# Performance work log

Measured on AMD Instinct MI355X. Metric: run time of the kernel, lower is better.

The kernel has to match this reference:

```python
import jax, jax.numpy as jnp
import numpy as np

V_THRESH = 0.3

@jax.custom_vjp
def spike(x):
    return (x > 0).astype(x.dtype)

def _spike_fwd(x):
    return spike(x), x

def _spike_bwd(x, g):
    # rectangular straight-through surrogate gradient (pass grad where |x| < 0.5)
    return (g * (jnp.abs(x) < 0.5).astype(g.dtype),)

spike.defvjp(_spike_fwd, _spike_bwd)


def setup_inputs() -> dict:
    key = jax.random.key(0)
    B, T, H = 128, 2048, 128
    k1, = jax.random.split(key, 1)
    x_seq = jax.random.normal(k1, (B, T, H), dtype=jnp.float32)
    v0 = jnp.zeros((B, H), dtype=jnp.float32)
    z0 = jnp.zeros((B, H), dtype=jnp.float32)
    decay_raw = jnp.zeros((H,), dtype=jnp.float32)  # nn.initializers.constant(0.0)
    return {"x_seq": x_seq, "v0": v0, "z0": z0, "decay_raw": decay_raw}


def reference(x_seq, v0, z0, decay_raw):
    # LIF recurrence: v_t = v_{t-1} * decay * (1 - z_{t-1}) + x_t ; z_t = spike(v_t - v_thresh)
    decay = jax.nn.sigmoid(decay_raw)  # (H,)

    def step(carry, x_t):
        v, z = carry
        v = v * decay * (1.0 - z) + x_t
        z_out = spike(v - V_THRESH)
        return (v, z_out), z_out

    x_tb = jnp.swapaxes(x_seq, 0, 1)  # [T, B, H] for lax.scan over time
    (_, _), spk_tb = jax.lax.scan(step, (v0, z0), x_tb)
    return jnp.swapaxes(spk_tb, 0, 1)  # [B, T, H]
```

## Files before the change

### kernel.cpp

```cpp
#include <hip/hip_runtime.h>
#include <math.h>


constexpr int Bdim = 128;
constexpr int Tdim = 2048;
constexpr int Hdim = 128;
constexpr int HW   = 64;
constexpr int U    = 128;
constexpr int XBUF = 4;
constexpr int NTILE = Tdim / U;
constexpr int NW   = 5;
constexpr float VTH = 0.3f;

typedef const __attribute__((address_space(1))) void* gptr_t;
typedef __attribute__((address_space(3))) void* lptr_t;

#define BAR() asm volatile("s_barrier" ::: "memory")

__global__ __launch_bounds__(NW * 64) void lif_kernel(
    const float* __restrict__ x,
    const float* __restrict__ v0,
    const float* __restrict__ z0,
    const float* __restrict__ decay_raw,
    float* __restrict__ out)
{
    __shared__ float xs[XBUF][U][HW];

    const int tid  = threadIdx.x;
    const int wave = tid >> 6;
    const int lane = tid & 63;
    const int blk  = blockIdx.x;
    const int b    = blk >> 1;
    const int h0   = (blk & 1) * HW;

    const float* xbase = x   + (size_t)b * Tdim * Hdim + h0;
    float*       obase = out + (size_t)b * Tdim * Hdim + h0;

    if (wave == 0) {
        const float decay = 1.0f / (1.0f + expf(-decay_raw[h0 + lane]));
        float v = v0[b * Hdim + h0 + lane];
        float z = z0[b * Hdim + h0 + lane];
        float* ol = obase + lane;

        BAR();

        for (int k = 0; k < NTILE; ++k) {
            const float (*xt)[HW] = xs[k & 3];
            float xa[8], xb[8], zb[8];
            #pragma unroll
            for (int j = 0; j < 8; ++j) xa[j] = xt[j][lane];

            #pragma unroll
            for (int bt = 0; bt < 16; ++bt) {
                if (bt < 15) {
                    #pragma unroll
                    for (int j = 0; j < 8; ++j) {
                        const float t = xt[(bt + 1) * 8 + j][lane];
                        if (bt & 1) xa[j] = t; else xb[j] = t;
                    }
                }
                #pragma unroll
                for (int j = 0; j < 8; ++j) {
                    const float xv = (bt & 1) ? xb[j] : xa[j];
                    const float vd = v * decay;
                    v = ((z > 0.5f) ? 0.0f : vd) + xv;
                    z = (v > VTH) ? 1.0f : 0.0f;
                    zb[j] = z;
                }
                const size_t t0 = (size_t)k * U + bt * 8;
                #pragma unroll
                for (int j = 0; j < 8; ++j)
                    ol[(t0 + j) * Hdim] = zb[j];
            }
            BAR();
        }
    } else {
        const int sub = (lane >> 4) * Hdim + (lane & 15) * 4;

        auto fill = [&](int tile, int buf) {
            const float* g = xbase + (size_t)tile * U * Hdim + sub;
            #pragma unroll
            for (int q = 0; q < 8; ++q) {
                const int jj = (wave - 1) * 8 + q;
                __builtin_amdgcn_global_load_lds(
                    (gptr_t)(const void*)(g + (size_t)(4 * jj) * Hdim),
                    (lptr_t)(void*)&xs[buf][4 * jj][0],
                    16, 0, 0);
            }
        };

        fill(0, 0); fill(1, 1); fill(2, 2);
        asm volatile("s_waitcnt vmcnt(16)" ::: "memory");
        BAR();

        for (int k = 0; k < NTILE; ++k) {
            if (k + 3 < NTILE) {
                fill(k + 3, (k + 3) & 3);
                asm volatile("s_waitcnt vmcnt(16)" ::: "memory");
            } else if (k == NTILE - 3) {
                asm volatile("s_waitcnt vmcnt(8)" ::: "memory");
            } else if (k == NTILE - 2) {
                asm volatile("s_waitcnt vmcnt(0)" ::: "memory");
            }
            BAR();
        }
    }
}

extern "C" void kernel_launch(void* const* d_in, const int* in_sizes, int n_in,
                              void* d_out, int out_size, void* d_ws, size_t ws_size,
                              hipStream_t stream) {
    const float* x         = (const float*)d_in[0];
    const float* v0        = (const float*)d_in[1];
    const float* z0        = (const float*)d_in[2];
    const float* decay_raw = (const float*)d_in[3];
    float* out = (float*)d_out;

    lif_kernel<<<Bdim * Hdim / HW, NW * 64, 0, stream>>>(x, v0, z0, decay_raw, out);
}
```

Before: 249.5 us.

## Offload spike stores to a writer wave via bit-packed LDS handoff

The compute wave no longer issues global stores. It packs each lane's spikes into 32-bit masks in LDS, and a dedicated third wave unpacks them and writes float4 rows to global memory one tile behind. Loading is consolidated into a single producer wave using 64-step tiles across six buffers, which shrinks the block from five waves to three. The aim is to take the scattered 4-byte output stores off the serial recurrence's critical path, at the cost of an extra LDS round-trip and a barrier per tile.

```diff
diff --git a/kernel.cpp b/kernel.cpp
--- a/kernel.cpp
+++ b/kernel.cpp
@@ -6,25 +6,23 @@
 constexpr int Tdim = 2048;
 constexpr int Hdim = 128;
 constexpr int HW   = 64;
-constexpr int U    = 128;
-constexpr int XBUF = 4;
-constexpr int NTILE = Tdim / U;
-constexpr int NW   = 5;
+constexpr int U    = 64;
+constexpr int NB   = 6;
+constexpr int NT   = Tdim / U;
 constexpr float VTH = 0.3f;
 
 typedef const __attribute__((address_space(1))) void* gptr_t;
 typedef __attribute__((address_space(3))) void* lptr_t;
 
-#define BAR() asm volatile("s_barrier" ::: "memory")
-
-__global__ __launch_bounds__(NW * 64) void lif_kernel(
+__global__ __launch_bounds__(192) void lif_kernel(
     const float* __restrict__ x,
     const float* __restrict__ v0,
     const float* __restrict__ z0,
     const float* __restrict__ decay_raw,
     float* __restrict__ out)
 {
-    __shared__ float xs[XBUF][U][HW];
+    __shared__ float    xs[NB][U][HW];
+    __shared__ unsigned zw[2][2][HW];
 
     const int tid  = threadIdx.x;
     const int wave = tid >> 6;
@@ -36,74 +34,94 @@
     const float* xbase = x   + (size_t)b * Tdim * Hdim + h0;
     float*       obase = out + (size_t)b * Tdim * Hdim + h0;
 
-    if (wave == 0) {
-        const float decay = 1.0f / (1.0f + expf(-decay_raw[h0 + lane]));
+    if (wave == 1) {
+        const int sub = (lane >> 4) * Hdim + (lane & 15) * 4;
+        auto fill = [&](int tile, int buf) {
+            const float* g = xbase + (size_t)tile * U * Hdim + sub;
+            #pragma unroll
+            for (int q = 0; q < 16; ++q)
+                __builtin_amdgcn_global_load_lds(
+                    (gptr_t)(const void*)(g + (size_t)(4 * q) * Hdim),
+                    (lptr_t)(void*)&xs[buf][4 * q][0], 16, 0, 0);
+        };
+        fill(0, 0); fill(1, 1); fill(2, 2);
+        asm volatile("s_waitcnt vmcnt(32)");
+        __builtin_amdgcn_s_barrier();
+        int buf = 3;
+        for (int k = 0; k < NT; ++k) {
+            if (k + 3 < NT) {
+                fill(k + 3, buf);
+                buf = (buf + 1 == NB) ? 0 : buf + 1;
+                asm volatile("s_waitcnt vmcnt(32)");
+            } else if (k == NT - 3) {
+                asm volatile("s_waitcnt vmcnt(16)");
+            } else if (k == NT - 2) {
+                asm volatile("s_waitcnt vmcnt(0)");
+            }
+            __builtin_amdgcn_s_barrier();
+        }
+    } else if (wave == 0) {
+        const float d = 1.0f / (1.0f + expf(-decay_raw[h0 + lane]));
         float v = v0[b * Hdim + h0 + lane];
         float z = z0[b * Hdim + h0 + lane];
-        float* ol = obase + lane;
+        __builtin_amdgcn_s_barrier();
 
-        BAR();
-
-        for (int k = 0; k < NTILE; ++k) {
-            const float (*xt)[HW] = xs[k & 3];
-            float xa[8], xb[8], zb[8];
+        int cb = 0;
+        for (int k = 0; k < NT; ++k) {
+            unsigned w0 = 0, w1 = 0;
+            float xa[16], xb[16];
             #pragma unroll
-            for (int j = 0; j < 8; ++j) xa[j] = xt[j][lane];
-
+            for (int j = 0; j < 16; ++j) xa[j] = xs[cb][j][lane];
             #pragma unroll
-            for (int bt = 0; bt < 16; ++bt) {
-                if (bt < 15) {
+            for (int bt = 0; bt < 4; ++bt) {
+                if (bt < 3) {
                     #pragma unroll
-                    for (int j = 0; j < 8; ++j) {
-                        const float t = xt[(bt + 1) * 8 + j][lane];
+                    for (int j = 0; j < 16; ++j) {
+                        const float t = xs[cb][(bt + 1) * 16 + j][lane];
                         if (bt & 1) xa[j] = t; else xb[j] = t;
                     }
                 }
                 #pragma unroll
-                for (int j = 0; j < 8; ++j) {
+                for (int j = 0; j < 16; ++j) {
                     const float xv = (bt & 1) ? xb[j] : xa[j];
-                    const float vd = v * decay;
+                    const float vd = v * d;
                     v = ((z > 0.5f) ? 0.0f : vd) + xv;
-                    z = (v > VTH) ? 1.0f : 0.0f;
-                    zb[j] = z;
+                    const bool s = v > VTH;
+                    z = s ? 1.0f : 0.0f;
+                    if (bt < 2) w0 |= s ? (1u << (bt * 16 + j))       : 0u;
+                    else        w1 |= s ? (1u << ((bt - 2) * 16 + j)) : 0u;
                 }
-                const size_t t0 = (size_t)k * U + bt * 8;
-                #pragma unroll
-                for (int j = 0; j < 8; ++j)
-                    ol[(t0 + j) * Hdim] = zb[j];
             }
-            BAR();
+            zw[k & 1][0][lane] = w0;
+            zw[k & 1][1][lane] = w1;
+            asm volatile("s_waitcnt lgkmcnt(0)");
+            __builtin_amdgcn_sched_barrier(0);
+            cb = (cb + 1 == NB) ? 0 : cb + 1;
+            __builtin_amdgcn_s_barrier();
         }
     } else {
-        const int sub = (lane >> 4) * Hdim + (lane & 15) * 4;
-
-        auto fill = [&](int tile, int buf) {
-            const float* g = xbase + (size_t)tile * U * Hdim + sub;
+        const int m  = lane & 15;
+        const int qt = lane >> 4;
+        auto flushtile = [&](int tt) {
+            const uint4 u = *(const uint4*)&zw[tt & 1][qt >> 1][4 * m];
+            float* o = obase + (size_t)(tt * U + qt * 16) * Hdim + 4 * m;
             #pragma unroll
-            for (int q = 0; q < 8; ++q) {
-                const int jj = (wave - 1) * 8 + q;
-                __builtin_amdgcn_global_load_lds(
-                    (gptr_t)(const void*)(g + (size_t)(4 * jj) * Hdim),
-                    (lptr_t)(void*)&xs[buf][4 * jj][0],
-                    16, 0, 0);
+            for (int i = 0; i < 16; ++i) {
+                const int bit = (qt & 1) * 16 + i;
+                float4 f;
+                f.x = ((u.x >> bit) & 1u) ? 1.0f : 0.0f;
+                f.y = ((u.y >> bit) & 1u) ? 1.0f : 0.0f;
+                f.z = ((u.z >> bit) & 1u) ? 1.0f : 0.0f;
+                f.w = ((u.w >> bit) & 1u) ? 1.0f : 0.0f;
+                *(float4*)(o + (size_t)i * Hdim) = f;
             }
         };
-
-        fill(0, 0); fill(1, 1); fill(2, 2);
-        asm volatile("s_waitcnt vmcnt(16)" ::: "memory");
-        BAR();
-
-        for (int k = 0; k < NTILE; ++k) {
-            if (k + 3 < NTILE) {
-                fill(k + 3, (k + 3) & 3);
-                asm volatile("s_waitcnt vmcnt(16)" ::: "memory");
-            } else if (k == NTILE - 3) {
-                asm volatile("s_waitcnt vmcnt(8)" ::: "memory");
-            } else if (k == NTILE - 2) {
-                asm volatile("s_waitcnt vmcnt(0)" ::: "memory");
-            }
-            BAR();
+        __builtin_amdgcn_s_barrier();
+        for (int k = 0; k < NT; ++k) {
+            if (k >= 1) flushtile(k - 1);
+            __builtin_amdgcn_s_barrier();
         }
+        flushtile(NT - 1);
     }
 }
 
@@ -116,5 +134,5 @@
     const float* decay_raw = (const float*)d_in[3];
     float* out = (float*)d_out;
 
-    lif_kernel<<<Bdim * Hdim / HW, NW * 64, 0, stream>>>(x, v0, z0, decay_raw, out);
+    lif_kernel<<<Bdim * Hdim / HW, 192, 0, stream>>>(x, v0, z0, decay_raw, out);
 }
```

New measurement: 241.7 us. 3.1% less time.
